# Optimization experiments

Measured on AMD Instinct MI355X. Metric: run time of the kernel, lower is better.

## Reference

```python
import jax, jax.numpy as jnp
import numpy as np

N_NODES = 100000
N_EDGES = 3200000
N_CH = 4  # n_channels_r
RESIDUE_TYPES_N = 20
FEATURES_DIM = 44


def _glorot(key, shape):
    fan_in, fan_out = shape[-2], shape[-1]
    lim = (6.0 / (fan_in + fan_out)) ** 0.5
    return jax.random.uniform(key, shape, jnp.float32, -lim, lim)


def setup_inputs() -> dict:
    key = jax.random.key(0)
    ks = jax.random.split(key, 24)
    inp = {
        "one_hot": jax.random.uniform(ks[0], (N_NODES, RESIDUE_TYPES_N), jnp.float32),
        "features": jax.random.normal(ks[1], (N_NODES, FEATURES_DIM), jnp.float32),
        "gemme_features": jax.random.normal(ks[2], (N_NODES, 1), jnp.float32),
        "edge_src": jax.random.randint(ks[3], (N_EDGES,), 0, N_NODES, jnp.int32),
        "edge_dst": jax.random.randint(ks[4], (N_EDGES,), 0, N_NODES, jnp.int32),
        "edge_weight": jax.random.uniform(ks[5], (N_CH, N_EDGES), jnp.float32),
    }
    dims = [RESIDUE_TYPES_N + FEATURES_DIM, 20, 16, 12, 8, 4]
    for i in range(5):
        inp[f"W{i+1}"] = _glorot(ks[6 + i], (N_CH, dims[i], dims[i + 1]))
        inp[f"b{i+1}"] = jnp.zeros((dims[i + 1],), jnp.float32)
    inp["lw1"] = _glorot(ks[12], (4, 8));  inp["lb1"] = jnp.zeros((8,), jnp.float32)
    inp["lw2"] = _glorot(ks[13], (8, 4));  inp["lb2"] = jnp.zeros((4,), jnp.float32)
    inp["lw3"] = _glorot(ks[14], (4, 1));  inp["lb3"] = jnp.zeros((1,), jnp.float32)
    return inp


def _gconv(x, src, dst, ew, W, b):
    # Multi-channel sparse graph conv: out = elu(sum_r (A_r @ x) @ W_r + b)
    n = x.shape[0]
    out = jnp.zeros((n, W.shape[2]), x.dtype)
    for r in range(W.shape[0]):  # small fixed channel count
        msg = x[src] * ew[r][:, None]                       # [E, in]
        agg = jax.ops.segment_sum(msg, dst, num_segments=n)  # [N, in]
        out = out + agg @ W[r]
    return jax.nn.elu(out + b)


def reference(one_hot, features, gemme_features, edge_src, edge_dst, edge_weight,
              W1, b1, W2, b2, W3, b3, W4, b4, W5, b5,
              lw1, lb1, lw2, lb2, lw3, lb3):
    x = jnp.concatenate([one_hot, features], axis=1)  # [N, 64]
    x = _gconv(x, edge_src, edge_dst, edge_weight, W1, b1)
    x = _gconv(x, edge_src, edge_dst, edge_weight, W2, b2)
    x = _gconv(x, edge_src, edge_dst, edge_weight, W3, b3)
    x = _gconv(x, edge_src, edge_dst, edge_weight, W4, b4)
    x = _gconv(x, edge_src, edge_dst, edge_weight, W5, b5)
    # dropout layers are identity in eval mode
    x = jax.nn.elu(x @ lw1 + lb1)
    x = jax.nn.elu(x @ lw2 + lb2)
    x = jax.nn.sigmoid(x @ lw3 + lb3)
    return x
```

## Files before the change

### kernel.cpp

```cpp
#include <hip/hip_runtime.h>
#include <hip/hip_bf16.h>
#include <cstdint>

#define DF(p) ((const float*)(p))
#define DI(p) ((const int*)(p))

typedef __attribute__((ext_vector_type(8))) short short8v;
typedef __attribute__((ext_vector_type(4))) float f32x4;
typedef __attribute__((ext_vector_type(2))) float f32x2;

static __device__ __forceinline__ float elu_f(float v){
  return v > 0.0f ? v : expm1f(v);
}
static __device__ __forceinline__ float bf_lo(unsigned u){
  union { unsigned u; float f; } c; c.u = u << 16; return c.f;
}
static __device__ __forceinline__ float bf_hi(unsigned u){
  union { unsigned u; float f; } c; c.u = u & 0xFFFF0000u; return c.f;
}
static __device__ __forceinline__ f32x2 bf2(unsigned u){
  union { unsigned u; float f; } lo, hi;
  lo.u = u << 16; hi.u = u & 0xFFFF0000u;
  return f32x2{lo.f, hi.f};
}
static __device__ __forceinline__ unsigned f2b(float f){
  union { float f; unsigned u; } c; c.f = f;
  return (c.u + 0x7FFFu + ((c.u >> 16) & 1u)) >> 16;
}
static __device__ __forceinline__ f32x2 pkfma(float w, f32x2 v, f32x2 c){
  return __builtin_elementwise_fma(f32x2{w, w}, v, c);
}
static __device__ __forceinline__ void acc_edge(
    uint2 u, uint2 wp,
    f32x2& L0, f32x2& H0, f32x2& L1, f32x2& H1,
    f32x2& L2, f32x2& H2, f32x2& L3, f32x2& H3){
  f32x2 vl = bf2(u.x), vh = bf2(u.y);
  float w0=bf_lo(wp.x), w1=bf_hi(wp.x), w2=bf_lo(wp.y), w3=bf_hi(wp.y);
  L0 = pkfma(w0, vl, L0); H0 = pkfma(w0, vh, H0);
  L1 = pkfma(w1, vl, L1); H1 = pkfma(w1, vh, H1);
  L2 = pkfma(w2, vl, L2); H2 = pkfma(w2, vh, H2);
  L3 = pkfma(w3, vl, L3); H3 = pkfma(w3, vh, H3);
}
template<int RL, int BND>
static __device__ __forceinline__ void wave_foldB(
    f32x2& a0, f32x2& a1, f32x2& a2, f32x2& a3,
    f32x2& a4, f32x2& a5, f32x2& a6, f32x2& a7){
  #pragma unroll
  for (int m = RL; m < BND; m <<= 1){
    a0.x += __shfl_xor(a0.x, m, 64); a0.y += __shfl_xor(a0.y, m, 64);
    a1.x += __shfl_xor(a1.x, m, 64); a1.y += __shfl_xor(a1.y, m, 64);
    a2.x += __shfl_xor(a2.x, m, 64); a2.y += __shfl_xor(a2.y, m, 64);
    a3.x += __shfl_xor(a3.x, m, 64); a3.y += __shfl_xor(a3.y, m, 64);
    a4.x += __shfl_xor(a4.x, m, 64); a4.y += __shfl_xor(a4.y, m, 64);
    a5.x += __shfl_xor(a5.x, m, 64); a5.y += __shfl_xor(a5.y, m, 64);
    a6.x += __shfl_xor(a6.x, m, 64); a6.y += __shfl_xor(a6.y, m, 64);
    a7.x += __shfl_xor(a7.x, m, 64); a7.y += __shfl_xor(a7.y, m, 64);
  }
}

#define NBLK_E 512
#define NBMAX  1024
#define CAP    4864

__global__ __launch_bounds__(256) void p1_bhist_kernel(
    const int* __restrict__ dst, int* __restrict__ cntB, int E, int NB){
  __shared__ int h[NBMAX];
  const int tid = threadIdx.x;
  for (int k = tid; k < NB; k += 256) h[k] = 0;
  __syncthreads();
  for (int e = blockIdx.x*256 + tid; e < E; e += NBLK_E*256)
    atomicAdd(&h[dst[e] >> 7], 1);
  __syncthreads();
  for (int k = tid; k < NB; k += 256) cntB[blockIdx.x*NBMAX + k] = h[k];
}

__global__ __launch_bounds__(256) void p2_bscan_kernel(
    int* __restrict__ cntB, int* __restrict__ btot, int NB){
  __shared__ int s[256];
  const int k = blockIdx.x;
  const int t = threadIdx.x;
  int v0 = cntB[(2*t  )*NBMAX + k];
  int v1 = cntB[(2*t+1)*NBMAX + k];
  int tsum = v0 + v1;
  s[t] = tsum;
  __syncthreads();
  for (int off = 1; off < 256; off <<= 1){
    int x = (t >= off) ? s[t - off] : 0;
    __syncthreads();
    s[t] += x;
    __syncthreads();
  }
  int excl = s[t] - tsum;
  cntB[(2*t  )*NBMAX + k] = excl;
  cntB[(2*t+1)*NBMAX + k] = excl + v0;
  if (t == 255) btot[k] = s[255];
}

__global__ __launch_bounds__(256) void p3_bscatter_kernel(
    const int* __restrict__ src, const int* __restrict__ dst,
    const float* __restrict__ ew,
    const int* __restrict__ cntB, const int* __restrict__ btot,
    int4* __restrict__ brec, int E, int NB){
  __shared__ int off_l[NBMAX];
  const int tid = threadIdx.x;
  for (int k = tid; k < NB; k += 256)
    off_l[k] = btot[k] + cntB[blockIdx.x*NBMAX + k];
  __syncthreads();
  for (int e = blockIdx.x*256 + tid; e < E; e += NBLK_E*256){
    int d = dst[e];
    unsigned a = f2b(ew[e])               | (f2b(ew[(size_t)E + e]) << 16);
    unsigned b = f2b(ew[2*(size_t)E + e]) | (f2b(ew[3*(size_t)E + e]) << 16);
    int pos = atomicAdd(&off_l[d >> 7], 1);
    brec[pos] = make_int4(src[e], (int)a, (int)b, d);
  }
}

__global__ __launch_bounds__(256) void p4_bsort_kernel(
    const int4* __restrict__ brec, const int* __restrict__ btot,
    int* __restrict__ csr_src, uint2* __restrict__ csr_w,
    int* __restrict__ rowptr, int E, int NB, int N){
  __shared__ int  h[128];
  __shared__ int  h2[128];
  __shared__ int  s[256];
  __shared__ int4 rec[CAP];
  const int k   = blockIdx.x;
  const int tid = threadIdx.x;
  const int beg = btot[k];
  const int end = (k + 1 < NB) ? btot[k + 1] : E;
  int count = end - beg;
  if (count > CAP) count = CAP;

  if (tid < 128) h[tid] = 0;
  __syncthreads();
  for (int t = tid; t < count; t += 256){
    int4 R = brec[beg + t];
    rec[t] = R;
    atomicAdd(&h[R.w & 127], 1);
  }
  __syncthreads();
  int v = (tid < 128) ? h[tid] : 0;
  s[tid] = v;
  __syncthreads();
  for (int off = 1; off < 256; off <<= 1){
    int x = (tid >= off) ? s[tid - off] : 0;
    __syncthreads();
    s[tid] += x;
    __syncthreads();
  }
  if (tid < 128){
    int excl = s[tid] - v;
    h2[tid] = excl;
    int idx = (k << 7) + tid;
    if (idx < N) rowptr[idx] = beg + excl;
  }
  if (k == 0 && tid == 128) rowptr[N] = E;
  __syncthreads();
  for (int t = tid; t < count; t += 256){
    int4 R = rec[t];
    int lp = atomicAdd(&h2[R.w & 127], 1);
    csr_src[beg + lp] = R.x;
    csr_w[beg + lp]   = make_uint2((unsigned)R.y, (unsigned)R.z);
  }
}


__global__ void hist_kernel(const int* __restrict__ dst, int* __restrict__ cnt,
                            int* __restrict__ rank, int E){
  int e = blockIdx.x*blockDim.x + threadIdx.x;
  if (e < E) rank[e] = atomicAdd(&cnt[dst[e]], 1);
}

__global__ void scatter_kernel(const int* __restrict__ src, const int* __restrict__ dst,
                               const int* __restrict__ rank, const int* __restrict__ rowptr,
                               int2* __restrict__ csr_se, int E){
  int e = blockIdx.x*blockDim.x + threadIdx.x;
  if (e >= E) return;
  int pos = rowptr[dst[e]] + rank[e];
  csr_se[pos] = make_int2(src[e], e);
}

__global__ void build_kernel(const int2* __restrict__ csr_se, const float* __restrict__ ew,
                             int* __restrict__ csr_src, uint2* __restrict__ csr_w, int E){
  int p = blockIdx.x*blockDim.x + threadIdx.x;
  if (p >= E) return;
  int2 se = csr_se[p];
  csr_src[p] = se.x;
  size_t e = (size_t)se.y;
  unsigned a = f2b(ew[e])               | (f2b(ew[(size_t)E + e]) << 16);
  unsigned b = f2b(ew[2*(size_t)E + e]) | (f2b(ew[3*(size_t)E + e]) << 16);
  csr_w[p] = make_uint2(a, b);
}

__global__ void scan1_kernel(int* __restrict__ data, int* __restrict__ bsum, int total){
  __shared__ int s[256];
  int i = blockIdx.x*256 + threadIdx.x;
  int v = (i < total) ? data[i] : 0;
  s[threadIdx.x] = v;
  __syncthreads();
  for (int off=1; off<256; off<<=1){
    int t = (threadIdx.x >= (unsigned)off) ? s[threadIdx.x - off] : 0;
    __syncthreads();
    s[threadIdx.x] += t;
    __syncthreads();
  }
  if (i < total) data[i] = s[threadIdx.x] - v;
  if (threadIdx.x == 255) bsum[blockIdx.x] = s[255];
}

__global__ void scan2_kernel(int* __restrict__ bsum, int nb){
  __shared__ int s[1024];
  int t = threadIdx.x;
  int v = (t < nb) ? bsum[t] : 0;
  s[t] = v;
  __syncthreads();
  for (int off=1; off<1024; off<<=1){
    int x = (t >= off) ? s[t - off] : 0;
    __syncthreads();
    s[t] += x;
    __syncthreads();
  }
  if (t < nb) bsum[t] = s[t] - v;
}

__global__ void scan3_kernel(int* __restrict__ rowptr, const int* __restrict__ bsum, int total){
  int i = blockIdx.x*256 + threadIdx.x;
  if (i < total) rowptr[i] += bsum[blockIdx.x];
}


static __device__ __forceinline__ void wtprep_one(
    const float* W, unsigned short* wtp, int t, int DIN, int DOUT, int XPI, int K){
  int j = t / K, k = t % K;
  int r = k / XPI, i = k % XPI;
  float v = (j < DOUT && i < XPI && i < DIN) ? W[(r*DIN + i)*DOUT + j] : 0.f;
  wtp[t] = (unsigned short)f2b(v);
}

__global__ __launch_bounds__(256) void wtprep_all_kernel(
    const float* __restrict__ W1, const float* __restrict__ W2,
    const float* __restrict__ W3, const float* __restrict__ W4,
    const float* __restrict__ W5,
    unsigned short* __restrict__ wtp1, unsigned short* __restrict__ wtp2,
    unsigned short* __restrict__ wtp3, unsigned short* __restrict__ wtp4,
    unsigned short* __restrict__ wtp5){
  int t = blockIdx.x*256 + threadIdx.x;
  if (t < 8192){ wtprep_one(W1, wtp1, t, 64, 20, 64, 256); return; }
  t -= 8192;
  if (t < 2048){ wtprep_one(W2, wtp2, t, 20, 16, 32, 128); return; }
  t -= 2048;
  if (t < 1024){ wtprep_one(W3, wtp3, t, 16, 12, 16, 64); return; }
  t -= 1024;
  if (t < 1024){ wtprep_one(W4, wtp4, t, 12, 8, 16, 64); return; }
  t -= 1024;
  if (t < 1024){ wtprep_one(W5, wtp5, t, 8, 4, 16, 64); return; }
}


__global__ __launch_bounds__(256) void concat_kernel(
    const float* __restrict__ oh, const float* __restrict__ f,
    unsigned short* __restrict__ xcat, int N){
  int i = blockIdx.x*256 + threadIdx.x;
  if (i >= N*64) return;
  int n = i >> 6, j = i & 63;
  float v = (j < 20) ? oh[n*20 + j] : f[n*44 + (j-20)];
  xcat[i] = (unsigned short)f2b(v);
}


template<int XPI, int NPW>
__global__ __launch_bounds__(256) void layerA_kernel(
    const int* __restrict__ rowptr, const int* __restrict__ csr_src,
    const uint2* __restrict__ csr_w, const unsigned short* __restrict__ x,
    unsigned short* __restrict__ z, int N)
{
  constexpr int RL   = XPI/4;
  constexpr int ES   = 64/RL;
  constexpr int NPB  = 4*NPW;
  constexpr int K    = 4*XPI;
  constexpr unsigned ROWB = RL*8;

  const int tid  = threadIdx.x;
  const int wave = tid >> 6;
  const int lane = tid & 63;
  const int sub  = lane / RL;
  const int q4   = lane & (RL - 1);
  const unsigned qoff = (unsigned)q4*8;
  const unsigned char* xb = (const unsigned char*)x;

  for (int t = 0; t < NPW; ++t){
    const int slot = wave*NPW + t;
    const int node = blockIdx.x*NPB + slot;
    if (node < N){
      const int beg = rowptr[node];
      const int end = rowptr[node+1];
      f32x2 AL0{0.f,0.f}, AL1{0.f,0.f}, AL2{0.f,0.f}, AL3{0.f,0.f};
      f32x2 AH0{0.f,0.f}, AH1{0.f,0.f}, AH2{0.f,0.f}, AH3{0.f,0.f};
      int k = beg;
      for (; k + 2*ES <= end; k += 2*ES){
        int kk0 = k + sub, kk1 = k + ES + sub;
        int s0 = csr_src[kk0], s1 = csr_src[kk1];
        uint2 wp0 = csr_w[kk0], wp1 = csr_w[kk1];
        uint2 u0 = *(const uint2*)(xb + ((unsigned)s0*ROWB + qoff));
        uint2 u1 = *(const uint2*)(xb + ((unsigned)s1*ROWB + qoff));
        acc_edge(u0, wp0, AL0, AH0, AL1, AH1, AL2, AH2, AL3, AH3);
        acc_edge(u1, wp1, AL0, AH0, AL1, AH1, AL2, AH2, AL3, AH3);
      }
      for (; k < end; k += ES){
        int kk = k + sub;
        int s = 0;
        uint2 wp = make_uint2(0u, 0u);
        if (kk < end){ s = csr_src[kk]; wp = csr_w[kk]; }
        uint2 u = *(const uint2*)(xb + ((unsigned)s*ROWB + qoff));
        acc_edge(u, wp, AL0, AH0, AL1, AH1, AL2, AH2, AL3, AH3);
      }
      wave_foldB<RL, 64>(AL0, AH0, AL1, AH1, AL2, AH2, AL3, AH3);
      if (sub == 0){
        uint2* zp = (uint2*)(z + (size_t)node*K);
        zp[0*RL + q4] = make_uint2(f2b(AL0.x) | (f2b(AL0.y)<<16), f2b(AH0.x) | (f2b(AH0.y)<<16));
        zp[1*RL + q4] = make_uint2(f2b(AL1.x) | (f2b(AL1.y)<<16), f2b(AH1.x) | (f2b(AH1.y)<<16));
        zp[2*RL + q4] = make_uint2(f2b(AL2.x) | (f2b(AL2.y)<<16), f2b(AH2.x) | (f2b(AH2.y)<<16));
        zp[3*RL + q4] = make_uint2(f2b(AL3.x) | (f2b(AL3.y)<<16), f2b(AH3.x) | (f2b(AH3.y)<<16));
      }
    }
  }
}


template<int K, int NJT, int DOUT, int XPO>
__global__ __launch_bounds__(256) void gemmB_kernel(
    const unsigned short* __restrict__ zbuf, const unsigned short* __restrict__ wtp,
    const float* __restrict__ bias, unsigned short* __restrict__ xout, int N)
{
  constexpr int RS   = K*2;
  constexpr int C16  = RS/16;
  constexpr int WT16 = NJT*16*C16;
  constexpr int ZT16 = 16*C16;
  __shared__ __align__(16) unsigned char wt[NJT*16*RS];
  __shared__ __align__(16) unsigned char zt[4][16*RS];

  const int tid  = threadIdx.x;
  const int wave = tid >> 6;
  const int lane = tid & 63;

  const uint4* wsrc = (const uint4*)wtp;
  for (int u = tid; u < WT16; u += 256){
    int row = u / C16, c = u % C16;
    *(uint4*)(wt + ((row*RS + c*16) ^ ((row & 7) << 4))) = wsrc[u];
  }
  const int node_base = (blockIdx.x*4 + wave)*16;
  const uint4* zsrc = (const uint4*)(zbuf + (size_t)node_base*K);
  for (int u = lane; u < ZT16; u += 64){
    int row = u / C16, c = u % C16;
    *(uint4*)(zt[wave] + ((row*RS + c*16) ^ ((row & 7) << 4))) = zsrc[u];
  }
  __syncthreads();

  const int rA = lane & 15;
  const int g  = lane >> 4;
  f32x4 acc[NJT];
  #pragma unroll
  for (int jt = 0; jt < NJT; ++jt) acc[jt] = f32x4{0.f, 0.f, 0.f, 0.f};

  #pragma unroll
  for (int ks = 0; ks < K/32; ++ks){
    short8v a = *(const short8v*)(zt[wave] + ((rA*RS + ks*64 + g*16) ^ ((rA & 7) << 4)));
    #pragma unroll
    for (int jt = 0; jt < NJT; ++jt){
      int rB = rA + jt*16;
      short8v bf = *(const short8v*)(wt + ((rB*RS + ks*64 + g*16) ^ ((rB & 7) << 4)));
      acc[jt] = __builtin_amdgcn_mfma_f32_16x16x32_bf16(a, bf, acc[jt], 0, 0, 0);
    }
  }

  #pragma unroll
  for (int jt = 0; jt < NJT; ++jt){
    int j = rA + jt*16;
    float bj = (j < DOUT) ? bias[j] : 0.f;
    #pragma unroll
    for (int r = 0; r < 4; ++r){
      int node = node_base + g*4 + r;
      if (node < N && j < XPO){
        float v = elu_f(acc[jt][r] + bj);
        xout[(size_t)node*XPO + j] = (unsigned short)f2b(v);
      }
    }
  }
}


template<int XPI, int NPW, int NJT, int DOUT, int XPO, int CLUST, bool FUSE_MLP>
__global__ __launch_bounds__(256) void fusedB_kernel(
    const int* __restrict__ rowptr, const int* __restrict__ csr_src,
    const uint2* __restrict__ csr_w, const unsigned short* __restrict__ x,
    const unsigned short* __restrict__ wtp, const float* __restrict__ bias,
    unsigned short* __restrict__ xout,
    const float* __restrict__ lw1, const float* __restrict__ lb1,
    const float* __restrict__ lw2, const float* __restrict__ lb2,
    const float* __restrict__ lw3, const float* __restrict__ lb3,
    float* __restrict__ mlp_out, int N)
{
  constexpr int RL   = XPI/4;
  constexpr int ES   = 64/RL;
  constexpr int NPB  = 4*NPW;
  constexpr int K    = 4*XPI;
  constexpr int KE   = K*CLUST;
  constexpr int RS   = KE*2;
  constexpr int C16  = RS/16;
  constexpr int C16B = (K*2)/16;
  constexpr int WT16 = NJT*16*C16;
  constexpr int SUBC = ES/CLUST;
  constexpr int BND  = RL*SUBC;
  constexpr unsigned ROWB = RL*8;
  __shared__ __align__(16) unsigned char wt[NJT*16*RS];
  __shared__ __align__(16) unsigned char zt[16*RS];

  const int tid  = threadIdx.x;
  const int wave = tid >> 6;
  const int lane = tid & 63;

  const uint4* wsrc = (const uint4*)wtp;
  for (int u = tid; u < WT16; u += 256){
    int row = u / C16, c = u % C16;
    *(uint4*)(wt + ((row*RS + c*16) ^ ((row & 7) << 4))) = wsrc[row*C16B + (c & (C16B - 1))];
  }

  const int sub = lane / RL;
  const int q4  = lane & (RL - 1);
  const unsigned qoff = (unsigned)q4*8;
  const unsigned char* xb = (const unsigned char*)x;
  const int node0 = blockIdx.x*NPB;

  for (int t = 0; t < NPW; ++t){
    const int slot = wave*NPW + t;
    const int node = node0 + slot;
    if (node < N){
      const int beg = rowptr[node];
      const int end = rowptr[node+1];
      f32x2 AL0{0.f,0.f}, AL1{0.f,0.f}, AL2{0.f,0.f}, AL3{0.f,0.f};
      f32x2 AH0{0.f,0.f}, AH1{0.f,0.f}, AH2{0.f,0.f}, AH3{0.f,0.f};
      int k = beg;
      for (; k + 2*ES <= end; k += 2*ES){
        int kk0 = k + sub, kk1 = k + ES + sub;
        int s0 = csr_src[kk0], s1 = csr_src[kk1];
        uint2 wp0 = csr_w[kk0], wp1 = csr_w[kk1];
        uint2 u0 = *(const uint2*)(xb + ((unsigned)s0*ROWB + qoff));
        uint2 u1 = *(const uint2*)(xb + ((unsigned)s1*ROWB + qoff));
        acc_edge(u0, wp0, AL0, AH0, AL1, AH1, AL2, AH2, AL3, AH3);
        acc_edge(u1, wp1, AL0, AH0, AL1, AH1, AL2, AH2, AL3, AH3);
      }
      for (; k < end; k += ES){
        int kk = k + sub;
        int s = 0;
        uint2 wp = make_uint2(0u, 0u);
        if (kk < end){ s = csr_src[kk]; wp = csr_w[kk]; }
        uint2 u = *(const uint2*)(xb + ((unsigned)s*ROWB + qoff));
        acc_edge(u, wp, AL0, AH0, AL1, AH1, AL2, AH2, AL3, AH3);
      }
      wave_foldB<RL, BND>(AL0, AH0, AL1, AH1, AL2, AH2, AL3, AH3);
      if ((sub & (SUBC - 1)) == 0){
        const int cid = sub / SUBC;
        uint2 c0 = make_uint2(f2b(AL0.x) | (f2b(AL0.y)<<16), f2b(AH0.x) | (f2b(AH0.y)<<16));
        uint2 c1 = make_uint2(f2b(AL1.x) | (f2b(AL1.y)<<16), f2b(AH1.x) | (f2b(AH1.y)<<16));
        uint2 c2 = make_uint2(f2b(AL2.x) | (f2b(AL2.y)<<16), f2b(AH2.x) | (f2b(AH2.y)<<16));
        uint2 c3 = make_uint2(f2b(AL3.x) | (f2b(AL3.y)<<16), f2b(AH3.x) | (f2b(AH3.y)<<16));
        const int sw = (slot & 7) << 4;
        const int kb = cid*K*2;
        int bc0 = kb + (0*XPI + q4*4)*2;
        int bc1 = kb + (1*XPI + q4*4)*2;
        int bc2 = kb + (2*XPI + q4*4)*2;
        int bc3 = kb + (3*XPI + q4*4)*2;
        *(uint2*)(zt + (((slot*RS + (bc0 & ~15)) ^ sw) + (bc0 & 15))) = c0;
        *(uint2*)(zt + (((slot*RS + (bc1 & ~15)) ^ sw) + (bc1 & 15))) = c1;
        *(uint2*)(zt + (((slot*RS + (bc2 & ~15)) ^ sw) + (bc2 & 15))) = c2;
        *(uint2*)(zt + (((slot*RS + (bc3 & ~15)) ^ sw) + (bc3 & 15))) = c3;
      }
    }
  }
  __syncthreads();

  if (wave == 0){
    const int rA = lane & 15;
    const int g  = lane >> 4;
    f32x4 acc[NJT];
    #pragma unroll
    for (int jt = 0; jt < NJT; ++jt) acc[jt] = f32x4{0.f, 0.f, 0.f, 0.f};

    #pragma unroll
    for (int ks = 0; ks < KE/32; ++ks){
      short8v a = *(const short8v*)(zt + ((rA*RS + ks*64 + g*16) ^ ((rA & 7) << 4)));
      #pragma unroll
      for (int jt = 0; jt < NJT; ++jt){
        int rB = rA + jt*16;
        short8v bf = *(const short8v*)(wt + ((rB*RS + ks*64 + g*16) ^ ((rB & 7) << 4)));
        acc[jt] = __builtin_amdgcn_mfma_f32_16x16x32_bf16(a, bf, acc[jt], 0, 0, 0);
      }
    }

    if (!FUSE_MLP){
      #pragma unroll
      for (int jt = 0; jt < NJT; ++jt){
        int j = rA + jt*16;
        float bj = (j < DOUT) ? bias[j] : 0.f;
        #pragma unroll
        for (int r = 0; r < 4; ++r){
          int row = g*4 + r;
          int node = node0 + row;
          if (row < NPB && node < N && j < XPO){
            float v = elu_f(acc[jt][r] + bj);
            xout[(size_t)node*XPO + j] = (unsigned short)f2b(v);
          }
        }
      }
    } else {
      float bj = (rA < DOUT) ? bias[rA] : 0.f;
      float val[4];
      #pragma unroll
      for (int r = 0; r < 4; ++r) val[r] = elu_f(acc[0][r] + bj);
      const int base = lane & 48;
      float x0 = 0.f, x1 = 0.f, x2 = 0.f, x3 = 0.f;
      #pragma unroll
      for (int q = 0; q < 4; ++q){
        float t0 = __shfl(val[q], base + 0, 64);
        float t1 = __shfl(val[q], base + 1, 64);
        float t2 = __shfl(val[q], base + 2, 64);
        float t3 = __shfl(val[q], base + 3, 64);
        if (rA == q){ x0 = t0; x1 = t1; x2 = t2; x3 = t3; }
      }
      if (rA < 4){
        int node = node0 + g*4 + rA;
        if (node < N){
          float xin[4] = {x0, x1, x2, x3};
          float h1[8];
          #pragma unroll
          for (int j = 0; j < 8; ++j){
            float a = lb1[j];
            #pragma unroll
            for (int i = 0; i < 4; ++i) a += xin[i]*lw1[i*8 + j];
            h1[j] = elu_f(a);
          }
          float h2[4];
          #pragma unroll
          for (int j = 0; j < 4; ++j){
            float a = lb2[j];
            #pragma unroll
            for (int i = 0; i < 8; ++i) a += h1[i]*lw2[i*4 + j];
            h2[j] = elu_f(a);
          }
          float a = lb3[0];
          #pragma unroll
          for (int i = 0; i < 4; ++i) a += h2[i]*lw3[i];
          mlp_out[node] = 1.0f / (1.0f + expf(-a));
        }
      }
    }
  }
}


__global__ __launch_bounds__(256) void mlp_kernel(
    const unsigned short* __restrict__ x,
    const float* __restrict__ lw1, const float* __restrict__ lb1,
    const float* __restrict__ lw2, const float* __restrict__ lb2,
    const float* __restrict__ lw3, const float* __restrict__ lb3,
    float* __restrict__ out, int N){
  int n = blockIdx.x*blockDim.x + threadIdx.x;
  if (n >= N) return;
  uint2 u = ((const uint2*)x)[n];
  float x0[4] = {bf_lo(u.x), bf_hi(u.x), bf_lo(u.y), bf_hi(u.y)};
  float h1[8];
  #pragma unroll
  for (int j=0;j<8;j++){
    float a = lb1[j];
    #pragma unroll
    for (int i=0;i<4;i++) a += x0[i]*lw1[i*8+j];
    h1[j] = elu_f(a);
  }
  float h2[4];
  #pragma unroll
  for (int j=0;j<4;j++){
    float a = lb2[j];
    #pragma unroll
    for (int i=0;i<8;i++) a += h1[i]*lw2[i*4+j];
    h2[j] = elu_f(a);
  }
  float a = lb3[0];
  #pragma unroll
  for (int i=0;i<4;i++) a += h2[i]*lw3[i];
  out[n] = 1.0f / (1.0f + expf(-a));
}


extern "C" void kernel_launch(void* const* d_in, const int* in_sizes, int n_in,
                              void* d_out, int out_size, void* d_ws, size_t ws_size,
                              hipStream_t stream){
  const float* one_hot  = DF(d_in[0]);
  const float* features = DF(d_in[1]);
  const int*   src      = DI(d_in[3]);
  const int*   dst      = DI(d_in[4]);
  const float* ew       = DF(d_in[5]);
  const float* W1 = DF(d_in[6]);  const float* b1 = DF(d_in[7]);
  const float* W2 = DF(d_in[8]);  const float* b2 = DF(d_in[9]);
  const float* W3 = DF(d_in[10]); const float* b3 = DF(d_in[11]);
  const float* W4 = DF(d_in[12]); const float* b4 = DF(d_in[13]);
  const float* W5 = DF(d_in[14]); const float* b5 = DF(d_in[15]);
  const float* lw1 = DF(d_in[16]); const float* lb1 = DF(d_in[17]);
  const float* lw2 = DF(d_in[18]); const float* lb2 = DF(d_in[19]);
  const float* lw3 = DF(d_in[20]); const float* lb3 = DF(d_in[21]);
  float* out = (float*)d_out;

  const int N = in_sizes[0] / 20;
  const int E = in_sizes[3];
  const int NB = (N + 127) >> 7;
  const int zN = ((N + 63)/64)*64;

  auto align = [](size_t x){ return (x + 255) & ~((size_t)255); };
  char* ws = (char*)d_ws;
  size_t off = 0;
  int*    rowptr  = (int*)(ws + off);    off = align(off + (size_t)(N+1)*4);
  int*    bsum    = (int*)(ws + off);    off = align(off + 4096);
  int*    csr_src = (int*)(ws + off);    off = align(off + (size_t)E*4);
  uint2*  csr_w   = (uint2*)(ws + off);  off = align(off + (size_t)E*8);
  unsigned short* wtp1 = (unsigned short*)(ws + off); off = align(off + 32*256*2);
  unsigned short* wtp2 = (unsigned short*)(ws + off); off = align(off + 16*128*2);
  unsigned short* wtp3 = (unsigned short*)(ws + off); off = align(off + 16*64*2);
  unsigned short* wtp4 = (unsigned short*)(ws + off); off = align(off + 16*64*2);
  unsigned short* wtp5 = (unsigned short*)(ws + off); off = align(off + 16*64*2);
  char*   regD    = ws + off;            off = align(off + (size_t)E*8);
  int2*   csr_se  = (int2*)regD;
  unsigned short* xcat = (unsigned short*)regD;
  char*   regE    = ws + off;            off = align(off + (size_t)E*4);
  int*    rank    = (int*)regE;
  unsigned short* xA = (unsigned short*)regE;
  unsigned short* xB = (unsigned short*)(ws + off); off = align(off + (size_t)N*16*2);
  unsigned short* xC = (unsigned short*)(ws + off); off = align(off + (size_t)N*16*2);
  char*   regF    = ws + off;
  size_t  off1 = align(off + (size_t)E*8);
  int*    cntB    = (int*)(ws + off1);   off1 = align(off1 + (size_t)NBLK_E*NBMAX*4);
  int*    btot    = (int*)(ws + off1);   off1 = align(off1 + (size_t)NBMAX*4);
  char*   regG    = ws + off1;
  int4*   brec    = (int4*)regG;
  size_t gsz = (size_t)E*16; if ((size_t)zN*512 > gsz) gsz = (size_t)zN*512;
  off1 = align(off1 + gsz);
  size_t  need_bucket = off1;

  const int TB = 256;
  const int nbE = (E + TB - 1) / TB;
  const int nbN = (N + TB - 1) / TB;
  const int total = N + 1;
  const int nb1 = (total + 255) / 256;
  const bool bucket_path = (ws_size >= need_bucket) && (NB <= NBMAX);
  unsigned short* zbuf = bucket_path ? (unsigned short*)regG : (unsigned short*)regF;

  wtprep_all_kernel<<<(13312 + 255)/256, TB, 0, stream>>>(
      W1, W2, W3, W4, W5, wtp1, wtp2, wtp3, wtp4, wtp5);

  if (bucket_path){
    p1_bhist_kernel<<<NBLK_E, TB, 0, stream>>>(dst, cntB, E, NB);
    p2_bscan_kernel<<<NB, TB, 0, stream>>>(cntB, btot, NB);
    scan2_kernel<<<1, 1024, 0, stream>>>(btot, NB);
    p3_bscatter_kernel<<<NBLK_E, TB, 0, stream>>>(src, dst, ew, cntB, btot, brec, E, NB);
    p4_bsort_kernel<<<NB, TB, 0, stream>>>(brec, btot, csr_src, csr_w, rowptr, E, NB, N);
  } else {
    hipMemsetAsync(rowptr, 0, (size_t)(N+1)*4, stream);
    hist_kernel<<<nbE, TB, 0, stream>>>(dst, rowptr, rank, E);
    scan1_kernel<<<nb1, 256, 0, stream>>>(rowptr, bsum, total);
    scan2_kernel<<<1, 1024, 0, stream>>>(bsum, nb1);
    scan3_kernel<<<nb1, 256, 0, stream>>>(rowptr, bsum, total);
    scatter_kernel<<<nbE, TB, 0, stream>>>(src, dst, rank, rowptr, csr_se, E);
    build_kernel<<<nbE, TB, 0, stream>>>(csr_se, ew, csr_src, csr_w, E);
  }

  concat_kernel<<<(N*64 + TB - 1)/TB, TB, 0, stream>>>(one_hot, features, xcat, N);

  const int NBB = (N + 63)/64;
  layerA_kernel<64,1><<<(N+3)/4, TB, 0, stream>>>(rowptr, csr_src, csr_w, xcat, zbuf, N);
  gemmB_kernel<256,2,20,32><<<NBB, TB, 0, stream>>>(zbuf, wtp1, b1, xA, N);
  fusedB_kernel<32,2,1,16,16,2,false><<<(N+7)/8,   TB, 0, stream>>>(
      rowptr, csr_src, csr_w, xA, wtp2, b2, xB,
      nullptr, nullptr, nullptr, nullptr, nullptr, nullptr, nullptr, N);
  fusedB_kernel<16,4,1,12,16,4,false><<<(N+15)/16, TB, 0, stream>>>(
      rowptr, csr_src, csr_w, xB, wtp3, b3, xC,
      nullptr, nullptr, nullptr, nullptr, nullptr, nullptr, nullptr, N);
  fusedB_kernel<16,4,1, 8,16,4,false><<<(N+15)/16, TB, 0, stream>>>(
      rowptr, csr_src, csr_w, xC, wtp4, b4, xA,
      nullptr, nullptr, nullptr, nullptr, nullptr, nullptr, nullptr, N);
  fusedB_kernel<16,4,1, 4, 4,4,true><<<(N+15)/16, TB, 0, stream>>>(
      rowptr, csr_src, csr_w, xA, wtp5, b5, nullptr,
      lw1, lb1, lw2, lb2, lw3, lb3, out, N);
}
```

Before: 435.7 us.

## Pack bucket records into 12 bytes and deepen edge-loop unrolling

Bucket scatter records shrink from a 16-byte int4 to a packed 4-byte src|local-dst word plus an 8-byte weight pair stored in separate arrays. This cuts scatter and sort traffic, with a guard restricting the path to N below 2^17. The layerA gather loop gains a 4-way unrolled edge loop and an unrolled node loop, and the fused kernel preloads its rowptr values into registers. The aim is more memory-level parallelism in the gathers, at the cost of higher register pressure.

```diff
diff --git a/kernel.cpp b/kernel.cpp
--- a/kernel.cpp
+++ b/kernel.cpp
@@ -100,7 +100,7 @@
     const int* __restrict__ src, const int* __restrict__ dst,
     const float* __restrict__ ew,
     const int* __restrict__ cntB, const int* __restrict__ btot,
-    int4* __restrict__ brec, int E, int NB){
+    unsigned* __restrict__ bsd, uint2* __restrict__ bw, int E, int NB){
   __shared__ int off_l[NBMAX];
   const int tid = threadIdx.x;
   for (int k = tid; k < NB; k += 256)
@@ -111,18 +111,21 @@
     unsigned a = f2b(ew[e])               | (f2b(ew[(size_t)E + e]) << 16);
     unsigned b = f2b(ew[2*(size_t)E + e]) | (f2b(ew[3*(size_t)E + e]) << 16);
     int pos = atomicAdd(&off_l[d >> 7], 1);
-    brec[pos] = make_int4(src[e], (int)a, (int)b, d);
+    bsd[pos] = (unsigned)src[e] | ((unsigned)(d & 127) << 17);
+    bw[pos]  = make_uint2(a, b);
   }
 }
 
 __global__ __launch_bounds__(256) void p4_bsort_kernel(
-    const int4* __restrict__ brec, const int* __restrict__ btot,
+    const unsigned* __restrict__ bsd, const uint2* __restrict__ bw,
+    const int* __restrict__ btot,
     int* __restrict__ csr_src, uint2* __restrict__ csr_w,
     int* __restrict__ rowptr, int E, int NB, int N){
-  __shared__ int  h[128];
-  __shared__ int  h2[128];
-  __shared__ int  s[256];
-  __shared__ int4 rec[CAP];
+  __shared__ int   h[128];
+  __shared__ int   h2[128];
+  __shared__ int   s[256];
+  __shared__ unsigned spd[CAP];
+  __shared__ uint2    spw[CAP];
   const int k   = blockIdx.x;
   const int tid = threadIdx.x;
   const int beg = btot[k];
@@ -133,9 +136,10 @@
   if (tid < 128) h[tid] = 0;
   __syncthreads();
   for (int t = tid; t < count; t += 256){
-    int4 R = brec[beg + t];
-    rec[t] = R;
-    atomicAdd(&h[R.w & 127], 1);
+    unsigned p = bsd[beg + t];
+    spd[t] = p;
+    spw[t] = bw[beg + t];
+    atomicAdd(&h[p >> 17], 1);
   }
   __syncthreads();
   int v = (tid < 128) ? h[tid] : 0;
@@ -156,10 +160,10 @@
   if (k == 0 && tid == 128) rowptr[N] = E;
   __syncthreads();
   for (int t = tid; t < count; t += 256){
-    int4 R = rec[t];
-    int lp = atomicAdd(&h2[R.w & 127], 1);
-    csr_src[beg + lp] = R.x;
-    csr_w[beg + lp]   = make_uint2((unsigned)R.y, (unsigned)R.z);
+    unsigned p = spd[t];
+    int lp = atomicAdd(&h2[p >> 17], 1);
+    csr_src[beg + lp] = (int)(p & 0x1FFFFu);
+    csr_w[beg + lp]   = spw[t];
   }
 }
 
@@ -287,6 +291,7 @@
   const unsigned qoff = (unsigned)q4*8;
   const unsigned char* xb = (const unsigned char*)x;
 
+  #pragma unroll
   for (int t = 0; t < NPW; ++t){
     const int slot = wave*NPW + t;
     const int node = blockIdx.x*NPB + slot;
@@ -296,6 +301,19 @@
       f32x2 AL0{0.f,0.f}, AL1{0.f,0.f}, AL2{0.f,0.f}, AL3{0.f,0.f};
       f32x2 AH0{0.f,0.f}, AH1{0.f,0.f}, AH2{0.f,0.f}, AH3{0.f,0.f};
       int k = beg;
+      for (; k + 4*ES <= end; k += 4*ES){
+        int kk0 = k + sub, kk1 = k + ES + sub, kk2 = k + 2*ES + sub, kk3 = k + 3*ES + sub;
+        int s0 = csr_src[kk0], s1 = csr_src[kk1], s2 = csr_src[kk2], s3 = csr_src[kk3];
+        uint2 wp0 = csr_w[kk0], wp1 = csr_w[kk1], wp2 = csr_w[kk2], wp3 = csr_w[kk3];
+        uint2 u0 = *(const uint2*)(xb + ((unsigned)s0*ROWB + qoff));
+        uint2 u1 = *(const uint2*)(xb + ((unsigned)s1*ROWB + qoff));
+        uint2 u2 = *(const uint2*)(xb + ((unsigned)s2*ROWB + qoff));
+        uint2 u3 = *(const uint2*)(xb + ((unsigned)s3*ROWB + qoff));
+        acc_edge(u0, wp0, AL0, AH0, AL1, AH1, AL2, AH2, AL3, AH3);
+        acc_edge(u1, wp1, AL0, AH0, AL1, AH1, AL2, AH2, AL3, AH3);
+        acc_edge(u2, wp2, AL0, AH0, AL1, AH1, AL2, AH2, AL3, AH3);
+        acc_edge(u3, wp3, AL0, AH0, AL1, AH1, AL2, AH2, AL3, AH3);
+      }
       for (; k + 2*ES <= end; k += 2*ES){
         int kk0 = k + sub, kk1 = k + ES + sub;
         int s0 = csr_src[kk0], s1 = csr_src[kk1];
@@ -430,12 +448,20 @@
   const unsigned char* xb = (const unsigned char*)x;
   const int node0 = blockIdx.x*NPB;
 
+  int rp[NPW + 1];
+  #pragma unroll
+  for (int i = 0; i <= NPW; ++i){
+    int idx = node0 + wave*NPW + i;
+    rp[i] = rowptr[idx > N ? N : idx];
+  }
+
+  #pragma unroll
   for (int t = 0; t < NPW; ++t){
     const int slot = wave*NPW + t;
     const int node = node0 + slot;
     if (node < N){
-      const int beg = rowptr[node];
-      const int end = rowptr[node+1];
+      const int beg = rp[t];
+      const int end = rp[t+1];
       f32x2 AL0{0.f,0.f}, AL1{0.f,0.f}, AL2{0.f,0.f}, AL3{0.f,0.f};
       f32x2 AH0{0.f,0.f}, AH1{0.f,0.f}, AH2{0.f,0.f}, AH3{0.f,0.f};
       int k = beg;
@@ -638,8 +664,9 @@
   int*    cntB    = (int*)(ws + off1);   off1 = align(off1 + (size_t)NBLK_E*NBMAX*4);
   int*    btot    = (int*)(ws + off1);   off1 = align(off1 + (size_t)NBMAX*4);
   char*   regG    = ws + off1;
-  int4*   brec    = (int4*)regG;
-  size_t gsz = (size_t)E*16; if ((size_t)zN*512 > gsz) gsz = (size_t)zN*512;
+  uint2*  bw      = (uint2*)regG;
+  unsigned* bsd   = (unsigned*)(regG + (size_t)E*8);
+  size_t gsz = (size_t)E*12; if ((size_t)zN*512 > gsz) gsz = (size_t)zN*512;
   off1 = align(off1 + gsz);
   size_t  need_bucket = off1;
 
@@ -648,7 +675,7 @@
   const int nbN = (N + TB - 1) / TB;
   const int total = N + 1;
   const int nb1 = (total + 255) / 256;
-  const bool bucket_path = (ws_size >= need_bucket) && (NB <= NBMAX);
+  const bool bucket_path = (ws_size >= need_bucket) && (NB <= NBMAX) && (N < (1 << 17));
   unsigned short* zbuf = bucket_path ? (unsigned short*)regG : (unsigned short*)regF;
 
   wtprep_all_kernel<<<(13312 + 255)/256, TB, 0, stream>>>(
@@ -658,8 +685,8 @@
     p1_bhist_kernel<<<NBLK_E, TB, 0, stream>>>(dst, cntB, E, NB);
     p2_bscan_kernel<<<NB, TB, 0, stream>>>(cntB, btot, NB);
     scan2_kernel<<<1, 1024, 0, stream>>>(btot, NB);
-    p3_bscatter_kernel<<<NBLK_E, TB, 0, stream>>>(src, dst, ew, cntB, btot, brec, E, NB);
-    p4_bsort_kernel<<<NB, TB, 0, stream>>>(brec, btot, csr_src, csr_w, rowptr, E, NB, N);
+    p3_bscatter_kernel<<<NBLK_E, TB, 0, stream>>>(src, dst, ew, cntB, btot, bsd, bw, E, NB);
+    p4_bsort_kernel<<<NB, TB, 0, stream>>>(bsd, bw, btot, csr_src, csr_w, rowptr, E, NB, N);
   } else {
     hipMemsetAsync(rowptr, 0, (size_t)(N+1)*4, stream);
     hist_kernel<<<nbE, TB, 0, stream>>>(dst, rowptr, rank, E);
```

Measured after the change: 456.8 us. +4.8%, slower.
